# Kernel optimization log

Hardware: AMD Instinct MI355X
Metric: run time of the kernel (lower is better)

Reference implementation:

```python
import jax, jax.numpy as jnp
import numpy as np
import math

DIM = 1024
MAX_SEQ_LEN = 8192

def setup_inputs() -> dict:
    key = jax.random.key(0)
    k1, k2, k3, k4 = jax.random.split(key, 4)
    x = jax.random.normal(k1, (4, 4096, DIM), dtype=jnp.float32)
    base_phases = jax.random.normal(k2, (MAX_SEQ_LEN, DIM), dtype=jnp.float32) * math.pi
    # nn.Linear(dim, dim): weight [out, in], bias [out]
    bound = 1.0 / math.sqrt(DIM)
    W = jax.random.uniform(k3, (DIM, DIM), dtype=jnp.float32, minval=-bound, maxval=bound)
    b = jax.random.uniform(k4, (DIM,), dtype=jnp.float32, minval=-bound, maxval=bound)
    return {"x": x, "base_phases": base_phases, "W": W, "b": b}

def reference(x, base_phases, W, b):
    B, L, D = x.shape
    phases = base_phases[:L][None, :, :]          # [1, L, D]
    value = jnp.einsum('bld,ed->ble', x, W) + b   # Linear: x @ W.T + b
    cos_p = jnp.cos(phases)
    sin_p = jnp.sin(phases)
    mem_real = jnp.cumsum(value * cos_p, axis=1)
    mem_imag = jnp.cumsum(value * sin_p, axis=1)
    retrieved = mem_real * cos_p + mem_imag * sin_p
    positions = jnp.arange(1, L + 1, dtype=jnp.float32)
    norm = jnp.sqrt(positions)[None, :, None]     # [1, L, 1]
    return retrieved / norm
```

## Files before the change

kernel.cpp:

```cpp
#include <hip/hip_runtime.h>
#include <hip/hip_bf16.h>

#define DIM 1024
#define SEQ 4096
#define NB 4
#define MROWS (NB * SEQ)
#define NC 64
#define CL (SEQ / NC)

#define BM 256
#define BN 256
#define BK 32
#define NTK 32
#define SLOTB 49152
#define GEMM_LDS (3 * SLOTB)

typedef __attribute__((ext_vector_type(8))) short bf16x8;
typedef __attribute__((ext_vector_type(4))) float f32x4;

static __device__ __forceinline__ unsigned short f2bf(float f) {
    union { float f; unsigned u; } v; v.f = f;
    unsigned r = v.u + 0x7FFF + ((v.u >> 16) & 1);
    return (unsigned short)(r >> 16);
}

static __device__ __forceinline__ float bf2f(unsigned short h) {
    union { unsigned u; float f; } v; v.u = ((unsigned)h) << 16;
    return v.f;
}

static __device__ __forceinline__ unsigned cvtpk(float a, float b) {
    unsigned r;
    asm("v_cvt_pk_bf16_f32 %0, %1, %2" : "=v"(r) : "v"(a), "v"(b));
    return r;
}

static __device__ __forceinline__ void gload_lds16(const void* g, void* l) {
    __builtin_amdgcn_global_load_lds((const __attribute__((address_space(1))) void*)g,
                                     (__attribute__((address_space(3))) void*)l, 16, 0, 0);
}

__global__ void convertW_kernel(const float* __restrict__ W, unsigned short* __restrict__ wb) {
    int t = blockIdx.x * 256 + threadIdx.x;
    float4 v = ((const float4*)W)[t];
    ushort4 o;
    o.x = f2bf(v.x); o.y = f2bf(v.y); o.z = f2bf(v.z); o.w = f2bf(v.w);
    ((ushort4*)wb)[t] = o;
}

static __device__ __forceinline__ void stage_Af32(const float* __restrict__ srcBase, char* smem,
                                                  int slot, int kt, int w, int lane) {
#pragma unroll
    for (int j = 0; j < 4; ++j) {
        const float* g = srcBase + (size_t)j * 8 * DIM + kt * BK;
        char* l = smem + (size_t)slot * SLOTB + (w * 4 + j) * 1024 + lane * 16;
        gload_lds16(g, l);
    }
}

static __device__ __forceinline__ void stage_B16(const unsigned short* __restrict__ srcBase, char* smem,
                                                 int slot, int kt, int w, int lane) {
#pragma unroll
    for (int r = 0; r < 2; ++r) {
        const unsigned short* g = srcBase + (size_t)r * 128 * DIM + kt * BK;
        char* l = smem + (size_t)slot * SLOTB + 32768 + (r * 128 + w * 16) * 64 + lane * 16;
        gload_lds16(g, l);
    }
}

__global__ __launch_bounds__(512, 2) void gemm_kernel(const float* __restrict__ X,
                                                      const unsigned short* __restrict__ Bm,
                                                      const float* __restrict__ bias,
                                                      unsigned short* __restrict__ V) {
    extern __shared__ char smem[];
    const int tid  = threadIdx.x;
    const int lane = tid & 63;
    const int w    = tid >> 6;
    const int wr   = (w >> 2) * 128;
    const int wc   = (w & 3) * 64;
    const int rl   = lane & 15;
    const int rh   = lane >> 4;
    const int m0   = blockIdx.x * BM;
    const int n0   = blockIdx.y * BN;

    const float* srcA = X + (size_t)(m0 + w * 32 + (lane >> 3)) * DIM + ((lane & 7) ^ (lane >> 3)) * 4;
    const unsigned short* srcB = Bm + (size_t)(n0 + w * 16 + (lane >> 2)) * DIM
                               + (((lane & 3) ^ ((lane >> 3) & 3)) * 8);

    const int swzB = (rh ^ ((rl >> 1) & 3)) * 16;
    const int aoff0 = (wr + rl) * 128 + (((rh * 2 + 0) ^ (rl & 7)) * 16);
    const int aoff1 = (wr + rl) * 128 + (((rh * 2 + 1) ^ (rl & 7)) * 16);

    f32x4 acc[8][4];
#pragma unroll
    for (int m = 0; m < 8; ++m)
#pragma unroll
        for (int n = 0; n < 4; ++n)
            acc[m][n] = (f32x4){0.f, 0.f, 0.f, 0.f};

    float4 bv4[4];
#pragma unroll
    for (int nf = 0; nf < 4; ++nf)
        bv4[nf] = *(const float4*)(bias + n0 + wc + nf * 16 + rh * 4);

    stage_Af32(srcA, smem, 0, 0, w, lane);
    stage_B16 (srcB, smem, 0, 0, w, lane);
    stage_Af32(srcA, smem, 1, 1, w, lane);
    stage_B16 (srcB, smem, 1, 1, w, lane);

#pragma unroll 1
    for (int t = 0; t < NTK; ++t) {
        asm volatile("s_waitcnt vmcnt(6)" ::: "memory");
        __builtin_amdgcn_s_barrier();
        const int sc = t % 3;
        const int ss = (t + 2) % 3;
        const int kn = (t + 2) & (NTK - 1);
        const char* sb = smem + (size_t)sc * SLOTB;

        bf16x8 bfr[4];
#pragma unroll
        for (int nf = 0; nf < 4; ++nf)
            bfr[nf] = *(const bf16x8*)(sb + 32768 + (wc + nf * 16 + rl) * 64 + swzB);

        bf16x8 af[4];
#pragma unroll
        for (int mf = 0; mf < 4; ++mf) {
            f32x4 q0 = *(const f32x4*)(sb + mf * 2048 + aoff0);
            f32x4 q1 = *(const f32x4*)(sb + mf * 2048 + aoff1);
            union { unsigned u[4]; bf16x8 v; } cv;
            cv.u[0] = cvtpk(q0[0], q0[1]); cv.u[1] = cvtpk(q0[2], q0[3]);
            cv.u[2] = cvtpk(q1[0], q1[1]); cv.u[3] = cvtpk(q1[2], q1[3]);
            af[mf] = cv.v;
        }
        stage_Af32(srcA, smem, ss, kn, w, lane);
        __builtin_amdgcn_s_setprio(1);
#pragma unroll
        for (int mf = 0; mf < 4; ++mf)
#pragma unroll
            for (int nf = 0; nf < 4; ++nf)
                acc[mf][nf] = __builtin_amdgcn_mfma_f32_16x16x32_bf16(bfr[nf], af[mf], acc[mf][nf], 0, 0, 0);
        __builtin_amdgcn_s_setprio(0);

#pragma unroll
        for (int mf = 0; mf < 4; ++mf) {
            f32x4 q0 = *(const f32x4*)(sb + (mf + 4) * 2048 + aoff0);
            f32x4 q1 = *(const f32x4*)(sb + (mf + 4) * 2048 + aoff1);
            union { unsigned u[4]; bf16x8 v; } cv;
            cv.u[0] = cvtpk(q0[0], q0[1]); cv.u[1] = cvtpk(q0[2], q0[3]);
            cv.u[2] = cvtpk(q1[0], q1[1]); cv.u[3] = cvtpk(q1[2], q1[3]);
            af[mf] = cv.v;
        }
        stage_B16(srcB, smem, ss, kn, w, lane);
        __builtin_amdgcn_s_setprio(1);
#pragma unroll
        for (int mf = 0; mf < 4; ++mf)
#pragma unroll
            for (int nf = 0; nf < 4; ++nf)
                acc[mf + 4][nf] = __builtin_amdgcn_mfma_f32_16x16x32_bf16(bfr[nf], af[mf], acc[mf + 4][nf], 0, 0, 0);
        __builtin_amdgcn_s_setprio(0);
    }

#pragma unroll
    for (int mf = 0; mf < 8; ++mf) {
        int grow = m0 + wr + mf * 16 + rl;
#pragma unroll
        for (int nf = 0; nf < 4; ++nf) {
            int gcol0 = n0 + wc + nf * 16 + rh * 4;
            ushort4 o;
            o.x = f2bf(acc[mf][nf][0] + bv4[nf].x);
            o.y = f2bf(acc[mf][nf][1] + bv4[nf].y);
            o.z = f2bf(acc[mf][nf][2] + bv4[nf].z);
            o.w = f2bf(acc[mf][nf][3] + bv4[nf].w);
            *(ushort4*)(V + (size_t)grow * DIM + gcol0) = o;
        }
    }
}

__global__ void passA_kernel(const unsigned short* __restrict__ val, const float* __restrict__ ph,
                             float* __restrict__ pr, float* __restrict__ pi) {
    int t  = blockIdx.x * 256 + threadIdx.x;
    int c  = blockIdx.y;
    int bb = blockIdx.z;
    const ushort2* v = (const ushort2*)val + ((size_t)bb * SEQ + (size_t)c * CL) * (DIM / 2) + t;
    const float2*  p = (const float2*)ph + (size_t)c * CL * (DIM / 2) + t;
    float sr0 = 0.f, si0 = 0.f, sr1 = 0.f, si1 = 0.f;
    for (int l = 0; l < CL; ++l) {
        ushort2 vv = v[(size_t)l * (DIM / 2)];
        float2  pp = p[(size_t)l * (DIM / 2)];
        float v0 = bf2f(vv.x), v1 = bf2f(vv.y);
        float s0, c0, s1, c1;
        __sincosf(pp.x, &s0, &c0);
        __sincosf(pp.y, &s1, &c1);
        sr0 += v0 * c0; si0 += v0 * s0;
        sr1 += v1 * c1; si1 += v1 * s1;
    }
    size_t idx = ((size_t)bb * NC + c) * DIM + 2 * t;
    pr[idx] = sr0; pr[idx + 1] = sr1;
    pi[idx] = si0; pi[idx + 1] = si1;
}

__global__ void passB_kernel(float* __restrict__ pr, float* __restrict__ pi) {
    int t = blockIdx.x * 256 + threadIdx.x;
    int bb = t >> 10;
    int e  = t & 1023;
    float r = 0.f, im = 0.f;
    for (int c = 0; c < NC; ++c) {
        size_t idx = ((size_t)bb * NC + c) * DIM + e;
        float tr = pr[idx], ti = pi[idx];
        pr[idx] = r; pi[idx] = im;
        r += tr; im += ti;
    }
}

__global__ void passC_kernel(const unsigned short* __restrict__ val, const float* __restrict__ ph,
                             const float* __restrict__ pr, const float* __restrict__ pi,
                             float* __restrict__ out) {
    int t  = blockIdx.x * 256 + threadIdx.x;
    int c  = blockIdx.y;
    int bb = blockIdx.z;
    size_t base = ((size_t)bb * SEQ + (size_t)c * CL) * (DIM / 2) + t;
    const ushort2* v = (const ushort2*)val + base;
    const float2*  p = (const float2*)ph + (size_t)c * CL * (DIM / 2) + t;
    float2* o = (float2*)out + base;
    size_t pidx = ((size_t)bb * NC + c) * DIM + 2 * t;
    float ar0 = pr[pidx], ar1 = pr[pidx + 1];
    float ai0 = pi[pidx], ai1 = pi[pidx + 1];
    const int l0 = c * CL;
    for (int l = 0; l < CL; ++l) {
        ushort2 vv = v[(size_t)l * (DIM / 2)];
        float2  pp = p[(size_t)l * (DIM / 2)];
        float v0 = bf2f(vv.x), v1 = bf2f(vv.y);
        float s0, c0, s1, c1;
        __sincosf(pp.x, &s0, &c0);
        __sincosf(pp.y, &s1, &c1);
        ar0 += v0 * c0; ai0 += v0 * s0;
        ar1 += v1 * c1; ai1 += v1 * s1;
        float rn = rsqrtf((float)(l0 + l + 1));
        float2 ov;
        ov.x = (ar0 * c0 + ai0 * s0) * rn;
        ov.y = (ar1 * c1 + ai1 * s1) * rn;
        o[(size_t)l * (DIM / 2)] = ov;
    }
}

extern "C" void kernel_launch(void* const* d_in, const int* in_sizes, int n_in,
                              void* d_out, int out_size, void* d_ws, size_t ws_size,
                              hipStream_t stream) {
    const float* x  = (const float*)d_in[0];
    const float* ph = (const float*)d_in[1];
    const float* W  = (const float*)d_in[2];
    const float* b  = (const float*)d_in[3];
    float* out = (float*)d_out;

    unsigned short* vb = (unsigned short*)d_ws;
    unsigned short* wb = vb + (size_t)MROWS * DIM;
    float* pr = (float*)(wb + (size_t)DIM * DIM);
    float* pi = pr + (size_t)NB * NC * DIM;

    (void)hipFuncSetAttribute((const void*)gemm_kernel,
                              hipFuncAttributeMaxDynamicSharedMemorySize, GEMM_LDS);

    convertW_kernel<<<DIM * DIM / 4 / 256, 256, 0, stream>>>(W, wb);
    {
        dim3 grid(MROWS / BM, DIM / BN);
        gemm_kernel<<<grid, 512, GEMM_LDS, stream>>>(x, wb, b, vb);
    }
    {
        dim3 grid(DIM / 512, NC, NB);
        passA_kernel<<<grid, 256, 0, stream>>>(vb, ph, pr, pi);
    }
    passB_kernel<<<16, 256, 0, stream>>>(pr, pi);
    {
        dim3 grid(DIM / 512, NC, NB);
        passC_kernel<<<grid, 256, 0, stream>>>(vb, ph, pr, pi, out);
    }
}
```

Baseline: 88.59 us.

## Fuse chunk partial-sum pass into GEMM epilogue

Removes the separate passA kernel. The GEMM epilogue now loads phases, computes sincos and accumulates per-chunk cos/sin weighted sums, using wavefront shuffles to reduce across rows, then writes the chunk partials directly. This avoids re-reading the bf16 value tensor and launching an extra kernel. In exchange the epilogue carries extra register pressure and a strided phase load, and each wave's 128-row tile has to line up with the 64-row chunks.

```diff
diff --git a/kernel.cpp b/kernel.cpp
--- a/kernel.cpp
+++ b/kernel.cpp
@@ -71,7 +71,10 @@
 __global__ __launch_bounds__(512, 2) void gemm_kernel(const float* __restrict__ X,
                                                       const unsigned short* __restrict__ Bm,
                                                       const float* __restrict__ bias,
-                                                      unsigned short* __restrict__ V) {
+                                                      const float* __restrict__ ph,
+                                                      unsigned short* __restrict__ V,
+                                                      float* __restrict__ pr,
+                                                      float* __restrict__ pi) {
     extern __shared__ char smem[];
     const int tid  = threadIdx.x;
     const int lane = tid & 63;
@@ -98,10 +101,10 @@
         for (int n = 0; n < 4; ++n)
             acc[m][n] = (f32x4){0.f, 0.f, 0.f, 0.f};
 
-    float4 bv4[4];
+    f32x4 bv4[4];
 #pragma unroll
     for (int nf = 0; nf < 4; ++nf)
-        bv4[nf] = *(const float4*)(bias + n0 + wc + nf * 16 + rh * 4);
+        bv4[nf] = *(const f32x4*)(bias + n0 + wc + nf * 16 + rh * 4);
 
     stage_Af32(srcA, smem, 0, 0, w, lane);
     stage_B16 (srcB, smem, 0, 0, w, lane);
@@ -160,43 +163,68 @@
         __builtin_amdgcn_s_setprio(0);
     }
 
+    const int bb = m0 >> 12;
+    const int lb = (m0 & (SEQ - 1)) + wr;
+    float csr[2][4][4], csi[2][4][4];
+#pragma unroll
+    for (int h = 0; h < 2; ++h)
+#pragma unroll
+        for (int nf = 0; nf < 4; ++nf)
+#pragma unroll
+            for (int j = 0; j < 4; ++j) { csr[h][nf][j] = 0.f; csi[h][nf][j] = 0.f; }
+
 #pragma unroll
     for (int mf = 0; mf < 8; ++mf) {
-        int grow = m0 + wr + mf * 16 + rl;
+        const int l    = lb + mf * 16 + rl;
+        const int grow = m0 + wr + mf * 16 + rl;
+        const int half = mf >> 2;
 #pragma unroll
         for (int nf = 0; nf < 4; ++nf) {
-            int gcol0 = n0 + wc + nf * 16 + rh * 4;
-            ushort4 o;
-            o.x = f2bf(acc[mf][nf][0] + bv4[nf].x);
-            o.y = f2bf(acc[mf][nf][1] + bv4[nf].y);
-            o.z = f2bf(acc[mf][nf][2] + bv4[nf].z);
-            o.w = f2bf(acc[mf][nf][3] + bv4[nf].w);
+            const int gcol0 = n0 + wc + nf * 16 + rh * 4;
+            f32x4 pp = *(const f32x4*)(ph + (size_t)l * DIM + gcol0);
+            unsigned short os[4];
+#pragma unroll
+            for (int j = 0; j < 4; ++j) {
+                float v = acc[mf][nf][j] + bv4[nf][j];
+                float s, cn;
+                __sincosf(pp[j], &s, &cn);
+                csr[half][nf][j] += v * cn;
+                csi[half][nf][j] += v * s;
+                os[j] = f2bf(v);
+            }
+            ushort4 o; o.x = os[0]; o.y = os[1]; o.z = os[2]; o.w = os[3];
             *(ushort4*)(V + (size_t)grow * DIM + gcol0) = o;
         }
     }
-}
-
-__global__ void passA_kernel(const unsigned short* __restrict__ val, const float* __restrict__ ph,
-                             float* __restrict__ pr, float* __restrict__ pi) {
-    int t  = blockIdx.x * 256 + threadIdx.x;
-    int c  = blockIdx.y;
-    int bb = blockIdx.z;
-    const ushort2* v = (const ushort2*)val + ((size_t)bb * SEQ + (size_t)c * CL) * (DIM / 2) + t;
-    const float2*  p = (const float2*)ph + (size_t)c * CL * (DIM / 2) + t;
-    float sr0 = 0.f, si0 = 0.f, sr1 = 0.f, si1 = 0.f;
-    for (int l = 0; l < CL; ++l) {
-        ushort2 vv = v[(size_t)l * (DIM / 2)];
-        float2  pp = p[(size_t)l * (DIM / 2)];
-        float v0 = bf2f(vv.x), v1 = bf2f(vv.y);
-        float s0, c0, s1, c1;
-        __sincosf(pp.x, &s0, &c0);
-        __sincosf(pp.y, &s1, &c1);
-        sr0 += v0 * c0; si0 += v0 * s0;
-        sr1 += v1 * c1; si1 += v1 * s1;
-    }
-    size_t idx = ((size_t)bb * NC + c) * DIM + 2 * t;
-    pr[idx] = sr0; pr[idx + 1] = sr1;
-    pi[idx] = si0; pi[idx + 1] = si1;
+#pragma unroll
+    for (int h = 0; h < 2; ++h)
+#pragma unroll
+        for (int nf = 0; nf < 4; ++nf)
+#pragma unroll
+            for (int j = 0; j < 4; ++j) {
+                float r = csr[h][nf][j], im = csi[h][nf][j];
+#pragma unroll
+                for (int mask = 1; mask < 16; mask <<= 1) {
+                    r  += __shfl_xor(r,  mask, 64);
+                    im += __shfl_xor(im, mask, 64);
+                }
+                csr[h][nf][j] = r; csi[h][nf][j] = im;
+            }
+    if (rl == 0) {
+#pragma unroll
+        for (int h = 0; h < 2; ++h) {
+            const int c = (lb + h * 64) >> 6;
+            const size_t base = ((size_t)bb * NC + c) * DIM;
+#pragma unroll
+            for (int nf = 0; nf < 4; ++nf) {
+                const int gcol0 = n0 + wc + nf * 16 + rh * 4;
+                *(float4*)(pr + base + gcol0) =
+                    (float4){csr[h][nf][0], csr[h][nf][1], csr[h][nf][2], csr[h][nf][3]};
+                *(float4*)(pi + base + gcol0) =
+                    (float4){csi[h][nf][0], csi[h][nf][1], csi[h][nf][2], csi[h][nf][3]};
+            }
+        }
+    }
 }
 
 __global__ void passB_kernel(float* __restrict__ pr, float* __restrict__ pi) {
@@ -263,11 +291,7 @@
     convertW_kernel<<<DIM * DIM / 4 / 256, 256, 0, stream>>>(W, wb);
     {
         dim3 grid(MROWS / BM, DIM / BN);
-        gemm_kernel<<<grid, 512, GEMM_LDS, stream>>>(x, wb, b, vb);
-    }
-    {
-        dim3 grid(DIM / 512, NC, NB);
-        passA_kernel<<<grid, 256, 0, stream>>>(vb, ph, pr, pi);
+        gemm_kernel<<<grid, 512, GEMM_LDS, stream>>>(x, wb, b, ph, vb, pr, pi);
     }
     passB_kernel<<<16, 256, 0, stream>>>(pr, pi);
     {
```

After: 85.78 us. 3.2% less time.
